# Optimization experiments

Measured on AMD Instinct MI355X. Metric: run time of the kernel, lower is better.

## Reference

```python
import jax, jax.numpy as jnp
import numpy as np

RANGE_EXTENDER = 5.0
EPS = 1e-8  # torch cosine_similarity eps

N_CLASSES = 256
LATENT = 256
H = W = 256


def setup_inputs() -> dict:
    key = jax.random.key(0)
    k1, k2, k3 = jax.random.split(key, 3)
    x = jax.random.normal(k1, (LATENT, H, W), dtype=jnp.float32)
    weights = jax.random.normal(k2, (N_CLASSES, LATENT), dtype=jnp.float32)
    scale = jax.random.normal(k3, (N_CLASSES,), dtype=jnp.float32)
    return {"x": x, "weights": weights, "scale": scale}


def reference(x, weights, scale):
    # out[c,i,j] = cos_sim(x[:,i,j], weights[c]) * scale[c] * RANGE_EXTENDER
    x_norm = jnp.sqrt(jnp.sum(x * x, axis=0, keepdims=True))           # (1, H, W)
    xn = x / jnp.maximum(x_norm, EPS)                                   # (D, H, W)
    w_norm = jnp.sqrt(jnp.sum(weights * weights, axis=1, keepdims=True))  # (C, 1)
    wn = weights / jnp.maximum(w_norm, EPS)                             # (C, D)
    cos = jnp.einsum("cd,dhw->chw", wn, xn)                            # (C, H, W)
    return cos * scale[:, None, None] * RANGE_EXTENDER
```

## Files before the change

### kernel.cpp

```cpp
#include <hip/hip_runtime.h>
#include <stdint.h>

typedef unsigned short u16;
typedef __bf16 bf16_t;
typedef bf16_t bf16x8 __attribute__((ext_vector_type(8)));
typedef float f32x4 __attribute__((ext_vector_type(4)));

static constexpr int P = 65536;

__device__ __forceinline__ float bfbits2f(uint32_t b) {
    union { uint32_t i; float f; } u; u.i = b << 16; return u.f;
}
__device__ __forceinline__ u16 f2bf(float f) {
    union { float f; uint32_t i; } u; u.f = f;
    uint32_t x = u.i + 0x7FFFu + ((u.i >> 16) & 1u);
    return (u16)(x >> 16);
}
__device__ __forceinline__ uint32_t pack2(float a, float b) {
    return (uint32_t)f2bf(a) | ((uint32_t)f2bf(b) << 16);
}

__device__ __forceinline__ int detect_bf16_input(const void* Xg) {
    const uint32_t* Xu = (const uint32_t*)Xg;
    const int lane = (int)(threadIdx.x & 63);
    const uint32_t v = Xu[(size_t)lane * 131071u];
    const uint32_t e = (v >> 7) & 0xFFu;
    unsigned long long m = __ballot(e >= 96u && e <= 135u);
    return __popcll(m) >= 40;
}

__global__ __launch_bounds__(64) void coshead_norms(
    const void* __restrict__ Xg, const void* __restrict__ Wg,
    const void* __restrict__ Sg, float* __restrict__ rs_ws)
{
    const int c    = (int)blockIdx.x;
    const int lane = (int)threadIdx.x;
    const int bf   = detect_bf16_input(Xg);
    float s;
    if (bf) {
        const uint2 v = *(const uint2*)((const u16*)Wg + (size_t)c * 256 + lane * 4);
        const float a = bfbits2f(v.x & 0xFFFFu), b = bfbits2f(v.x >> 16);
        const float d = bfbits2f(v.y & 0xFFFFu), e = bfbits2f(v.y >> 16);
        s = a * a + b * b + d * d + e * e;
    } else {
        const f32x4 v = *(const f32x4*)((const float*)Wg + (size_t)c * 256 + lane * 4);
        s = v[0] * v[0] + v[1] * v[1] + v[2] * v[2] + v[3] * v[3];
    }
    s += __shfl_xor(s, 1);  s += __shfl_xor(s, 2);  s += __shfl_xor(s, 4);
    s += __shfl_xor(s, 8);  s += __shfl_xor(s, 16); s += __shfl_xor(s, 32);
    if (lane == 0) {
        const float sc = bf ? bfbits2f((uint32_t)((const u16*)Sg)[c])
                            : ((const float*)Sg)[c];
        rs_ws[c] = sc * 5.0f / fmaxf(sqrtf(s), 1e-8f);
    }
}

__global__ __launch_bounds__(256, 3) void coshead_gemm(
    const void* __restrict__ Xg_, const void* __restrict__ Wg_,
    const float* __restrict__ rs_ws, float* __restrict__ Og)
{
    __shared__ char smem_[32768 + 8192];
    char* sA = smem_;
    char* sB = smem_ + 32768;

    const int t  = (int)threadIdx.x;
    const int l  = t & 63;
    const int w  = t >> 6;
    const int p0 = (int)blockIdx.x * 64;
    const int bf = detect_bf16_input(Xg_);

    const int g    = t & 7;
    const int r    = t >> 3;
    const int m16  = l & 15;
    const int quad = l >> 4;

    float ssq[8];
#pragma unroll
    for (int j = 0; j < 8; ++j) ssq[j] = 0.f;
    f32x4 acc[4][4];
#pragma unroll
    for (int a = 0; a < 4; ++a)
#pragma unroll
        for (int b = 0; b < 4; ++b)
#pragma unroll
            for (int i = 0; i < 4; ++i) acc[a][b][i] = 0.f;

    for (int kc = 0; kc < 4; ++kc) {
        if (bf) {
#pragma unroll
            for (int i = 0; i < 8; ++i) {
                const int row = i * 32 + r;
                const uint4 v = *(const uint4*)((const u16*)Wg_ + (size_t)row * 256 + kc * 64 + g * 8);
                *(uint4*)(sA + row * 128 + ((g ^ (row & 7)) * 16)) = v;
            }
            const u16* xp = (const u16*)Xg_ + (size_t)(2 * r + kc * 64) * P + p0 + g * 8;
            const uint4 v0 = *(const uint4*)xp;
            const uint4 v1 = *(const uint4*)(xp + P);
            const uint32_t e0[4] = {v0.x, v0.y, v0.z, v0.w};
            const uint32_t e1[4] = {v1.x, v1.y, v1.z, v1.w};
#pragma unroll
            for (int d = 0; d < 4; ++d) {
                const float f00 = bfbits2f(e0[d] & 0xFFFFu), f01 = bfbits2f(e0[d] >> 16);
                const float f10 = bfbits2f(e1[d] & 0xFFFFu), f11 = bfbits2f(e1[d] >> 16);
                ssq[2 * d]     += f00 * f00 + f10 * f10;
                ssq[2 * d + 1] += f01 * f01 + f11 * f11;
                const uint32_t d0 = (e0[d] & 0xFFFFu) | (e1[d] << 16);
                const uint32_t d1 = (e0[d] >> 16) | (e1[d] & 0xFFFF0000u);
                const int pj0 = g * 8 + 2 * d, pj1 = pj0 + 1;
                *(uint32_t*)(sB + pj0 * 128 + (((r >> 2) ^ (pj0 & 7) ^ g) * 16) + (r & 3) * 4) = d0;
                *(uint32_t*)(sB + pj1 * 128 + (((r >> 2) ^ (pj1 & 7) ^ g) * 16) + (r & 3) * 4) = d1;
            }
        } else {
#pragma unroll
            for (int i = 0; i < 8; ++i) {
                const int row = i * 32 + r;
                const float* wp = (const float*)Wg_ + (size_t)row * 256 + kc * 64 + g * 8;
                const f32x4 a = *(const f32x4*)wp;
                const f32x4 b = *(const f32x4*)(wp + 4);
                uint4 o;
                o.x = pack2(a[0], a[1]); o.y = pack2(a[2], a[3]);
                o.z = pack2(b[0], b[1]); o.w = pack2(b[2], b[3]);
                *(uint4*)(sA + row * 128 + ((g ^ (row & 7)) * 16)) = o;
            }
            const float* xp = (const float*)Xg_ + (size_t)(2 * r + kc * 64) * P + p0 + g * 8;
            const f32x4 c0  = *(const f32x4*)xp;
            const f32x4 c1  = *(const f32x4*)(xp + 4);
            const f32x4 d0v = *(const f32x4*)(xp + P);
            const f32x4 d1v = *(const f32x4*)(xp + P + 4);
            const float f0[8] = {c0[0], c0[1], c0[2], c0[3], c1[0], c1[1], c1[2], c1[3]};
            const float f1[8] = {d0v[0], d0v[1], d0v[2], d0v[3], d1v[0], d1v[1], d1v[2], d1v[3]};
#pragma unroll
            for (int j = 0; j < 8; ++j) {
                ssq[j] += f0[j] * f0[j] + f1[j] * f1[j];
                const int pix = g * 8 + j;
                *(uint32_t*)(sB + pix * 128 + (((r >> 2) ^ (pix & 7) ^ g) * 16) + (r & 3) * 4) =
                    pack2(f0[j], f1[j]);
            }
        }
        __syncthreads();
#pragma unroll
        for (int kk = 0; kk < 2; ++kk) {
            bf16x8 af[4], bfr[4];
#pragma unroll
            for (int tm = 0; tm < 4; ++tm) {
                const int row = w * 64 + tm * 16 + m16;
                af[tm] = *(const bf16x8*)(sA + row * 128 + (((kk * 4 + quad) ^ (row & 7)) * 16));
            }
#pragma unroll
            for (int tn = 0; tn < 4; ++tn) {
                const int pix = tn * 16 + m16;
                bfr[tn] = *(const bf16x8*)(sB + pix * 128 +
                           (((kk * 4 + quad) ^ (pix & 7) ^ (pix >> 3)) * 16));
            }
#pragma unroll
            for (int tm = 0; tm < 4; ++tm)
#pragma unroll
                for (int tn = 0; tn < 4; ++tn)
                    acc[tm][tn] = __builtin_amdgcn_mfma_f32_16x16x32_bf16(
                        af[tm], bfr[tn], acc[tm][tn], 0, 0, 0);
        }
        __syncthreads();
    }

    float* xs   = (float*)sA;
    float* xinv = (float*)sB;
#pragma unroll
    for (int j = 0; j < 8; ++j) xs[r * 64 + g * 8 + j] = ssq[j];
    __syncthreads();
    if (t < 64) {
        float sx = 0.f;
#pragma unroll
        for (int rr = 0; rr < 32; ++rr) sx += xs[rr * 64 + t];
        xinv[t] = 1.0f / fmaxf(sqrtf(sx), 1e-8f);
    }
    __syncthreads();

#pragma unroll
    for (int tn = 0; tn < 4; ++tn) {
        const float inv = xinv[tn * 16 + m16];
#pragma unroll
        for (int tm = 0; tm < 4; ++tm) {
            const int cbase = w * 64 + tm * 16 + quad * 4;
            const f32x4 rs4 = *(const f32x4*)(rs_ws + cbase);
#pragma unroll
            for (int i = 0; i < 4; ++i) {
                Og[(size_t)(cbase + i) * P + p0 + tn * 16 + m16] =
                    acc[tm][tn][i] * rs4[i] * inv;
            }
        }
    }
}

extern "C" void kernel_launch(void* const* d_in, const int* in_sizes, int n_in,
                              void* d_out, int out_size, void* d_ws, size_t ws_size,
                              hipStream_t stream) {
    (void)out_size; (void)ws_size;
    const void* X = d_in[0];
    const void* W = d_in[1];
    const void* S = d_in[2];
    for (int i = 0; i < n_in; ++i) {
        if (in_sizes[i] == 256 * 65536) X = d_in[i];
        else if (in_sizes[i] == 256 * 256) W = d_in[i];
        else if (in_sizes[i] == 256)      S = d_in[i];
    }
    float* rs = (float*)d_ws;
    coshead_norms<<<dim3(256), dim3(64), 0, stream>>>(X, W, S, rs);
    coshead_gemm<<<dim3(1024), dim3(256), 0, stream>>>(X, W, rs, (float*)d_out);
}
```

Measured before the change: 138.0 us.

## Pre-convert weights to bf16 and read A fragments directly from global/L2

The prep kernel now also writes a bf16 copy of the weights into the workspace. The GEMM kernel reads its A-operand MFMA fragments straight from that global copy instead of staging 32KB of weights through LDS each k-chunk. This cuts shared memory to 16KB, which allows occupancy 4, and the X tile in LDS is double-buffered so one barrier per chunk can be dropped. The fp32 X loads are also prefetched one chunk ahead in registers. The cost is per-wave global loads of weight fragments that are uncoalesced across rows and depend on L2 hits.

```diff
diff --git a/kernel.cpp b/kernel.cpp
--- a/kernel.cpp
+++ b/kernel.cpp
@@ -29,23 +29,29 @@
     return __popcll(m) >= 40;
 }
 
-__global__ __launch_bounds__(64) void coshead_norms(
+__global__ __launch_bounds__(64) void coshead_prep(
     const void* __restrict__ Xg, const void* __restrict__ Wg,
-    const void* __restrict__ Sg, float* __restrict__ rs_ws)
+    const void* __restrict__ Sg, float* __restrict__ rs_ws,
+    u16* __restrict__ wbf)
 {
     const int c    = (int)blockIdx.x;
     const int lane = (int)threadIdx.x;
     const int bf   = detect_bf16_input(Xg);
     float s;
+    uint2 packed;
     if (bf) {
         const uint2 v = *(const uint2*)((const u16*)Wg + (size_t)c * 256 + lane * 4);
         const float a = bfbits2f(v.x & 0xFFFFu), b = bfbits2f(v.x >> 16);
         const float d = bfbits2f(v.y & 0xFFFFu), e = bfbits2f(v.y >> 16);
         s = a * a + b * b + d * d + e * e;
+        packed = v;
     } else {
         const f32x4 v = *(const f32x4*)((const float*)Wg + (size_t)c * 256 + lane * 4);
         s = v[0] * v[0] + v[1] * v[1] + v[2] * v[2] + v[3] * v[3];
-    }
+        packed.x = pack2(v[0], v[1]);
+        packed.y = pack2(v[2], v[3]);
+    }
+    *(uint2*)(wbf + (size_t)c * 256 + lane * 4) = packed;
     s += __shfl_xor(s, 1);  s += __shfl_xor(s, 2);  s += __shfl_xor(s, 4);
     s += __shfl_xor(s, 8);  s += __shfl_xor(s, 16); s += __shfl_xor(s, 32);
     if (lane == 0) {
@@ -55,13 +61,11 @@
     }
 }
 
-__global__ __launch_bounds__(256, 3) void coshead_gemm(
-    const void* __restrict__ Xg_, const void* __restrict__ Wg_,
+__global__ __launch_bounds__(256, 4) void coshead_gemm(
+    const void* __restrict__ Xg_, const u16* __restrict__ Wbf,
     const float* __restrict__ rs_ws, float* __restrict__ Og)
 {
-    __shared__ char smem_[32768 + 8192];
-    char* sA = smem_;
-    char* sB = smem_ + 32768;
+    __shared__ char smem_[16384];
 
     const int t  = (int)threadIdx.x;
     const int l  = t & 63;
@@ -85,14 +89,20 @@
 #pragma unroll
             for (int i = 0; i < 4; ++i) acc[a][b][i] = 0.f;
 
+    f32x4 rA, rB, rC, rD;
+    if (!bf) {
+        const float* xp = (const float*)Xg_ + (size_t)(2 * r) * P + p0 + g * 8;
+        rA = *(const f32x4*)xp;
+        rB = *(const f32x4*)(xp + 4);
+        rC = *(const f32x4*)(xp + P);
+        rD = *(const f32x4*)(xp + P + 4);
+    }
+
+    const u16* wrow = Wbf + (size_t)(w * 64 + m16) * 256 + quad * 8;
+
     for (int kc = 0; kc < 4; ++kc) {
+        char* sBw = smem_ + (kc & 1) * 8192;
         if (bf) {
-#pragma unroll
-            for (int i = 0; i < 8; ++i) {
-                const int row = i * 32 + r;
-                const uint4 v = *(const uint4*)((const u16*)Wg_ + (size_t)row * 256 + kc * 64 + g * 8);
-                *(uint4*)(sA + row * 128 + ((g ^ (row & 7)) * 16)) = v;
-            }
             const u16* xp = (const u16*)Xg_ + (size_t)(2 * r + kc * 64) * P + p0 + g * 8;
             const uint4 v0 = *(const uint4*)xp;
             const uint4 v1 = *(const uint4*)(xp + P);
@@ -107,49 +117,40 @@
                 const uint32_t d0 = (e0[d] & 0xFFFFu) | (e1[d] << 16);
                 const uint32_t d1 = (e0[d] >> 16) | (e1[d] & 0xFFFF0000u);
                 const int pj0 = g * 8 + 2 * d, pj1 = pj0 + 1;
-                *(uint32_t*)(sB + pj0 * 128 + (((r >> 2) ^ (pj0 & 7) ^ g) * 16) + (r & 3) * 4) = d0;
-                *(uint32_t*)(sB + pj1 * 128 + (((r >> 2) ^ (pj1 & 7) ^ g) * 16) + (r & 3) * 4) = d1;
+                *(uint32_t*)(sBw + pj0 * 128 + (((r >> 2) ^ (pj0 & 7) ^ g) * 16) + (r & 3) * 4) = d0;
+                *(uint32_t*)(sBw + pj1 * 128 + (((r >> 2) ^ (pj1 & 7) ^ g) * 16) + (r & 3) * 4) = d1;
             }
         } else {
-#pragma unroll
-            for (int i = 0; i < 8; ++i) {
-                const int row = i * 32 + r;
-                const float* wp = (const float*)Wg_ + (size_t)row * 256 + kc * 64 + g * 8;
-                const f32x4 a = *(const f32x4*)wp;
-                const f32x4 b = *(const f32x4*)(wp + 4);
-                uint4 o;
-                o.x = pack2(a[0], a[1]); o.y = pack2(a[2], a[3]);
-                o.z = pack2(b[0], b[1]); o.w = pack2(b[2], b[3]);
-                *(uint4*)(sA + row * 128 + ((g ^ (row & 7)) * 16)) = o;
-            }
-            const float* xp = (const float*)Xg_ + (size_t)(2 * r + kc * 64) * P + p0 + g * 8;
-            const f32x4 c0  = *(const f32x4*)xp;
-            const f32x4 c1  = *(const f32x4*)(xp + 4);
-            const f32x4 d0v = *(const f32x4*)(xp + P);
-            const f32x4 d1v = *(const f32x4*)(xp + P + 4);
-            const float f0[8] = {c0[0], c0[1], c0[2], c0[3], c1[0], c1[1], c1[2], c1[3]};
-            const float f1[8] = {d0v[0], d0v[1], d0v[2], d0v[3], d1v[0], d1v[1], d1v[2], d1v[3]};
+            const float f0[8] = {rA[0], rA[1], rA[2], rA[3], rB[0], rB[1], rB[2], rB[3]};
+            const float f1[8] = {rC[0], rC[1], rC[2], rC[3], rD[0], rD[1], rD[2], rD[3]};
 #pragma unroll
             for (int j = 0; j < 8; ++j) {
                 ssq[j] += f0[j] * f0[j] + f1[j] * f1[j];
                 const int pix = g * 8 + j;
-                *(uint32_t*)(sB + pix * 128 + (((r >> 2) ^ (pix & 7) ^ g) * 16) + (r & 3) * 4) =
+                *(uint32_t*)(sBw + pix * 128 + (((r >> 2) ^ (pix & 7) ^ g) * 16) + (r & 3) * 4) =
                     pack2(f0[j], f1[j]);
+            }
+            if (kc < 3) {
+                const float* xp = (const float*)Xg_ + (size_t)(2 * r + (kc + 1) * 64) * P + p0 + g * 8;
+                rA = *(const f32x4*)xp;
+                rB = *(const f32x4*)(xp + 4);
+                rC = *(const f32x4*)(xp + P);
+                rD = *(const f32x4*)(xp + P + 4);
             }
         }
         __syncthreads();
+
+        const u16* wk = wrow + kc * 64;
 #pragma unroll
         for (int kk = 0; kk < 2; ++kk) {
             bf16x8 af[4], bfr[4];
 #pragma unroll
-            for (int tm = 0; tm < 4; ++tm) {
-                const int row = w * 64 + tm * 16 + m16;
-                af[tm] = *(const bf16x8*)(sA + row * 128 + (((kk * 4 + quad) ^ (row & 7)) * 16));
-            }
+            for (int tm = 0; tm < 4; ++tm)
+                af[tm] = *(const bf16x8*)(wk + tm * 16 * 256 + kk * 32);
 #pragma unroll
             for (int tn = 0; tn < 4; ++tn) {
                 const int pix = tn * 16 + m16;
-                bfr[tn] = *(const bf16x8*)(sB + pix * 128 +
+                bfr[tn] = *(const bf16x8*)(sBw + pix * 128 +
                            (((kk * 4 + quad) ^ (pix & 7) ^ (pix >> 3)) * 16));
             }
 #pragma unroll
@@ -159,11 +160,11 @@
                     acc[tm][tn] = __builtin_amdgcn_mfma_f32_16x16x32_bf16(
                         af[tm], bfr[tn], acc[tm][tn], 0, 0, 0);
         }
-        __syncthreads();
-    }
-
-    float* xs   = (float*)sA;
-    float* xinv = (float*)sB;
+    }
+
+    __syncthreads();
+    float* xs   = (float*)smem_;
+    float* xinv = (float*)(smem_ + 8192);
 #pragma unroll
     for (int j = 0; j < 8; ++j) xs[r * 64 + g * 8 + j] = ssq[j];
     __syncthreads();
@@ -175,17 +176,19 @@
     }
     __syncthreads();
 
-#pragma unroll
-    for (int tn = 0; tn < 4; ++tn) {
-        const float inv = xinv[tn * 16 + m16];
-#pragma unroll
-        for (int tm = 0; tm < 4; ++tm) {
-            const int cbase = w * 64 + tm * 16 + quad * 4;
-            const f32x4 rs4 = *(const f32x4*)(rs_ws + cbase);
+    float inv4[4];
+#pragma unroll
+    for (int tn = 0; tn < 4; ++tn) inv4[tn] = xinv[tn * 16 + m16];
+#pragma unroll
+    for (int tm = 0; tm < 4; ++tm) {
+        const int cbase = w * 64 + tm * 16 + quad * 4;
+        const f32x4 rs4 = *(const f32x4*)(rs_ws + cbase);
+#pragma unroll
+        for (int tn = 0; tn < 4; ++tn) {
 #pragma unroll
             for (int i = 0; i < 4; ++i) {
                 Og[(size_t)(cbase + i) * P + p0 + tn * 16 + m16] =
-                    acc[tm][tn][i] * rs4[i] * inv;
+                    acc[tm][tn][i] * rs4[i] * inv4[tn];
             }
         }
     }
@@ -203,7 +206,8 @@
         else if (in_sizes[i] == 256 * 256) W = d_in[i];
         else if (in_sizes[i] == 256)      S = d_in[i];
     }
-    float* rs = (float*)d_ws;
-    coshead_norms<<<dim3(256), dim3(64), 0, stream>>>(X, W, S, rs);
-    coshead_gemm<<<dim3(1024), dim3(256), 0, stream>>>(X, W, rs, (float*)d_out);
-}
+    float* rs  = (float*)d_ws;
+    u16*   wbf = (u16*)((char*)d_ws + 1024);
+    coshead_prep<<<dim3(256), dim3(64), 0, stream>>>(X, W, S, rs, wbf);
+    coshead_gemm<<<dim3(1024), dim3(256), 0, stream>>>(X, wbf, rs, (float*)d_out);
+}
```

Result: slower. 179.3 us (+29.9%).
